# Optimization experiments

Hardware: AMD Instinct MI355X
Metric: run time of the kernel (lower is better)

## Reference

```python
import jax, jax.numpy as jnp
import numpy as np

D_MODEL = 768
N_HEADS = 12
HEAD_DIM = D_MODEL // N_HEADS


def setup_inputs() -> dict:
    key = jax.random.key(0)
    ks = jax.random.split(key, 9)
    s = 1.0 / np.sqrt(D_MODEL)
    return {
        "x": jax.random.normal(ks[0], (2, 2048, D_MODEL), dtype=jnp.float32),
        "Wq": jax.random.uniform(ks[1], (D_MODEL, D_MODEL), minval=-s, maxval=s, dtype=jnp.float32),
        "bq": jax.random.uniform(ks[2], (D_MODEL,), minval=-s, maxval=s, dtype=jnp.float32),
        "Wk": jax.random.uniform(ks[3], (D_MODEL, D_MODEL), minval=-s, maxval=s, dtype=jnp.float32),
        "bk": jax.random.uniform(ks[4], (D_MODEL,), minval=-s, maxval=s, dtype=jnp.float32),
        "Wv": jax.random.uniform(ks[5], (D_MODEL, D_MODEL), minval=-s, maxval=s, dtype=jnp.float32),
        "bv": jax.random.uniform(ks[6], (D_MODEL,), minval=-s, maxval=s, dtype=jnp.float32),
        "Wo": jax.random.uniform(ks[7], (D_MODEL, D_MODEL), minval=-s, maxval=s, dtype=jnp.float32),
        "bo": jax.random.uniform(ks[8], (D_MODEL,), minval=-s, maxval=s, dtype=jnp.float32),
    }


def reference(x, Wq, bq, Wk, bk, Wv, bv, Wo, bo):
    B, S, D = x.shape
    H, Hd = N_HEADS, HEAD_DIM
    # nn.Linear: y = x @ W.T + b
    q = (x @ Wq.T + bq).reshape(B, S, H, Hd).transpose(0, 2, 1, 3)  # [B,H,S,Hd]
    k = (x @ Wk.T + bk).reshape(B, S, H, Hd).transpose(0, 2, 1, 3)
    v = (x @ Wv.T + bv).reshape(B, S, H, Hd).transpose(0, 2, 1, 3)
    scores = jnp.einsum('bhqd,bhkd->bhqk', q, k) / np.sqrt(Hd)  # [B,H,S,S]
    attn = jax.nn.softmax(scores, axis=-1)
    out = jnp.einsum('bhqk,bhkd->bhqd', attn, v)  # [B,H,S,Hd]
    out = out.transpose(0, 2, 1, 3).reshape(B, S, D)
    return out @ Wo.T + bo
```

## Files before the change

### kernel.cpp

```cpp
#include <hip/hip_runtime.h>

#define D_MODEL 768
#define SEQ 2048
#define BATCH 2
#define NHEADS 12
#define HDIM 64
#define M_TOTAL (BATCH*SEQ)
#define NQK (2*D_MODEL)

typedef __attribute__((ext_vector_type(8))) short short8;
typedef __attribute__((ext_vector_type(4))) short short4_t;
typedef __attribute__((ext_vector_type(4))) float floatx4;

#define MFMA_PV(a,b,c) __builtin_amdgcn_mfma_f32_16x16x16bf16_1k(a,b,c,0,0,0)
#define EXP2(x) __builtin_amdgcn_exp2f(x)

static __device__ __forceinline__ unsigned short f2bf(float f) {
    union { float f; unsigned int u; } v; v.f = f;
    unsigned int r = (v.u + 0x7fffu + ((v.u >> 16) & 1u)) >> 16;
    return (unsigned short)r;
}

static __device__ __forceinline__ void async16(void* lds, const void* g) {
    __builtin_amdgcn_global_load_lds(
        (const __attribute__((address_space(1))) unsigned int*)g,
        (__attribute__((address_space(3))) unsigned int*)lds, 16, 0, 0);
}

#define X8    393216
#define W8    73728
#define CVT_N (X8 + 4*W8)
#define CVT_BLOCKS (CVT_N/256 + 6)
__global__ __launch_bounds__(256) void cvt_all_kernel(
    const float* __restrict__ x,  const float* __restrict__ Wq,
    const float* __restrict__ Wk, const float* __restrict__ Wv,
    const float* __restrict__ Wo, const float* __restrict__ bq,
    const float* __restrict__ bk,
    unsigned short* __restrict__ xb, unsigned short* __restrict__ wqk,
    unsigned short* __restrict__ wvb, unsigned short* __restrict__ wob,
    float* __restrict__ bqk)
{
    int i = blockIdx.x * 256 + threadIdx.x;
    if (i >= CVT_N) {
        int j = i - CVT_N;
        if (j < 1536) bqk[j] = (j < 768) ? bq[j] : bk[j - 768];
        return;
    }
    const float* src; unsigned short* dst;
    if (i < X8)             { src = x  + (size_t)i*8;            dst = xb  + (size_t)i*8; }
    else if (i < X8 + W8)   { int j = i - X8;          src = Wq + (size_t)j*8; dst = wqk + (size_t)j*8; }
    else if (i < X8 + 2*W8) { int j = i - (X8 + W8);   src = Wk + (size_t)j*8; dst = wqk + 589824 + (size_t)j*8; }
    else if (i < X8 + 3*W8) { int j = i - (X8 + 2*W8); src = Wv + (size_t)j*8; dst = wvb + (size_t)j*8; }
    else                    { int j = i - (X8 + 3*W8); src = Wo + (size_t)j*8; dst = wob + (size_t)j*8; }
    const float4* s = (const float4*)src;
    float4 a = s[0], b = s[1];
    short8 o;
    o[0]=(short)f2bf(a.x); o[1]=(short)f2bf(a.y); o[2]=(short)f2bf(a.z); o[3]=(short)f2bf(a.w);
    o[4]=(short)f2bf(b.x); o[5]=(short)f2bf(b.y); o[6]=(short)f2bf(b.z); o[7]=(short)f2bf(b.w);
    *(short8*)dst = o;
}

template<int MI>
__device__ __forceinline__ void gemm_core_db(
    const unsigned short* __restrict__ A, const unsigned short* __restrict__ W,
    int m0, int n0, unsigned short* smem, floatx4 (&acc)[MI][4], int t)
{
    const int ASZ = MI*32*64;
    const int BSZ = ASZ + 8192;
    const int quad = (t >> 4) & 3, l = t & 15;
    const int wvv = t >> 6, wr = wvv >> 1, wc = wvv & 1;
    const int base_off = t & ~63;

    auto stage = [&](int buf, int kt) {
        char* AsB = (char*)(smem + buf*BSZ);
        char* WsB = (char*)(smem + buf*BSZ + ASZ);
#pragma unroll
        for (int it = 0; it < MI; ++it) {
            int slot = it*256 + t;
            int r = slot >> 3, c = (slot & 7) ^ (r & 7);
            async16(AsB + (size_t)(it*256 + base_off)*16, A + (size_t)(m0+r)*768 + kt*64 + c*8);
        }
#pragma unroll
        for (int it = 0; it < 4; ++it) {
            int slot = it*256 + t;
            int r = slot >> 3, c = (slot & 7) ^ (r & 7);
            async16(WsB + (size_t)(it*256 + base_off)*16, W + (size_t)(n0+r)*768 + kt*64 + c*8);
        }
    };

    stage(0, 0);
    for (int kt = 0; kt < 12; ++kt) {
        __syncthreads();
        if (kt < 11) stage((kt+1)&1, kt+1);
        const char* AsB = (const char*)(smem + (kt&1)*BSZ);
        const char* WsB = (const char*)(smem + (kt&1)*BSZ + ASZ);
#pragma unroll
        for (int ks = 0; ks < 2; ++ks) {
            short8 af[MI], wf[4];
#pragma unroll
            for (int mi = 0; mi < MI; ++mi) {
                int m = wr*(MI*16) + mi*16 + l;
                af[mi] = *(const short8*)(AsB + m*128 + (((ks*4+quad) ^ (m&7))*16));
            }
#pragma unroll
            for (int ni = 0; ni < 4; ++ni) {
                int n = wc*64 + ni*16 + l;
                wf[ni] = *(const short8*)(WsB + n*128 + (((ks*4+quad) ^ (n&7))*16));
            }
#pragma unroll
            for (int mi = 0; mi < MI; ++mi)
#pragma unroll
                for (int ni = 0; ni < 4; ++ni)
                    acc[mi][ni] = __builtin_amdgcn_mfma_f32_16x16x32_bf16(
                        af[mi], wf[ni], acc[mi][ni], 0, 0, 0);
        }
    }
}

__global__ __launch_bounds__(256) void gemm_qkvt_kernel(
    const unsigned short* __restrict__ xb, const unsigned short* __restrict__ wqk,
    const unsigned short* __restrict__ wvb,
    const float* __restrict__ bqk, const float* __restrict__ bv,
    unsigned short* __restrict__ qkout, unsigned short* __restrict__ vtout)
{
    __shared__ unsigned short smem[2*16384];
    const int t = threadIdx.x;
    int bid = blockIdx.x;
    const bool isqk = bid < 384;
    const unsigned short *A, *W; int m0, n0;
    if (isqk) { A = xb;  W = wqk; m0 = (bid/12)*128; n0 = (bid%12)*128; }
    else { int v = bid - 384; A = wvb; W = xb; m0 = (v%6)*128; n0 = (v/6)*128; }

    floatx4 acc[4][4];
#pragma unroll
    for (int i=0;i<4;i++)
#pragma unroll
        for (int j=0;j<4;j++) acc[i][j] = (floatx4){0.f,0.f,0.f,0.f};

    gemm_core_db<4>(A, W, m0, n0, smem, acc, t);

    const int lane = t & 63, quad = lane >> 4, l = lane & 15;
    const int wvv = t >> 6, wr = wvv >> 1, wc = wvv & 1;

    __syncthreads();
#pragma unroll
    for (int mi=0;mi<4;mi++)
#pragma unroll
        for (int ni=0;ni<4;ni++) {
            int col = wc*64 + ni*16 + l;
            float bcol = isqk ? bqk[n0 + col] : 0.f;
#pragma unroll
            for (int r=0;r<4;r++) {
                int row = wr*64 + mi*16 + quad*4 + r;
                float bb = isqk ? bcol : bv[m0 + row];
                smem[row*128 + col] = f2bf(acc[mi][ni][r] + bb);
            }
        }
    __syncthreads();
#pragma unroll
    for (int i=0;i<8;i++) {
        int slot = i*256 + t;
        int r = slot >> 4, c = slot & 15;
        if (isqk) {
            short8 val = *(const short8*)(smem + r*128 + c*8);
            *(short8*)(qkout + (size_t)(m0+r)*NQK + n0 + c*8) = val;
        } else {
            int kb32 = (c >> 2)*32 + (c & 3)*4;
            short4_t lo = *(const short4_t*)(smem + r*128 + kb32);
            short4_t hi = *(const short4_t*)(smem + r*128 + kb32 + 16);
            short8 val;
            val[0]=lo[0]; val[1]=lo[1]; val[2]=lo[2]; val[3]=lo[3];
            val[4]=hi[0]; val[5]=hi[1]; val[6]=hi[2]; val[7]=hi[3];
            int f = m0 + r, tok = n0 + c*8;
            *(short8*)(vtout + ((size_t)(tok>>11)*768 + f)*SEQ + (tok & (SEQ-1))) = val;
        }
    }
}

__global__ __launch_bounds__(256) void gemm_out_kernel(
    const unsigned short* __restrict__ ab, const unsigned short* __restrict__ wob,
    const float* __restrict__ bo, float* __restrict__ out)
{
    __shared__ unsigned short smem[2*12288];
    const int t = threadIdx.x;
    int bid = blockIdx.x;
    int m0 = (bid/6)*64, n0 = (bid%6)*128;

    floatx4 acc[2][4];
#pragma unroll
    for (int i=0;i<2;i++)
#pragma unroll
        for (int j=0;j<4;j++) acc[i][j] = (floatx4){0.f,0.f,0.f,0.f};

    gemm_core_db<2>(ab, wob, m0, n0, smem, acc, t);

    const int lane = t & 63, quad = lane >> 4, l = lane & 15;
    const int wvv = t >> 6, wr = wvv >> 1, wc = wvv & 1;
#pragma unroll
    for (int mi=0;mi<2;mi++)
#pragma unroll
        for (int ni=0;ni<4;ni++) {
            int col = n0 + wc*64 + ni*16 + l;
            float bb = bo[col];
#pragma unroll
            for (int r=0;r<4;r++) {
                int row = m0 + wr*32 + mi*16 + quad*4 + r;
                out[(size_t)row*768 + col] = acc[mi][ni][r] + bb;
            }
        }
}

__global__ __launch_bounds__(256) void attn_kernel(
    const unsigned short* __restrict__ qk,
    const unsigned short* __restrict__ vt,
    unsigned short* __restrict__ aout)
{
    __shared__ unsigned short Ks[128*64];
    __shared__ unsigned short Vs[64*128];
    char* KsB = (char*)Ks; char* VsB = (char*)Vs;
    const int t = threadIdx.x;
    const int lane = t & 63, w = t >> 6;
    const int l16 = lane & 15, quad = lane >> 4;
    const int q0 = blockIdx.x * 64;
    const int h = blockIdx.y, b = blockIdx.z;
    const size_t rowbase = (size_t)b * SEQ;
    const size_t vbase = ((size_t)(b*NHEADS + h))*HDIM*SEQ;
    const int base_off = t & ~63;

    short8 qf0, qf1;
    {
        const unsigned short* qr = qk + (rowbase + q0 + w*16 + l16)*NQK + h*64;
        qf0 = *(const short8*)(qr + quad*8);
        qf1 = *(const short8*)(qr + 32 + quad*8);
    }

    floatx4 oacc[4];
#pragma unroll
    for (int i=0;i<4;i++) oacc[i] = (floatx4){0.f,0.f,0.f,0.f};
    float lsum = 0.f;
    short4_t pf[8];

    const float C1 = 0.18033688011112042f;
    const float C2 = -4.32808512266689f;

    for (int kt = 0; kt < SEQ/128; ++kt) {
        __syncthreads();
#pragma unroll
        for (int it = 0; it < 4; ++it) {
            int slot = it*256 + t;
            int r = slot >> 3, c = (slot & 7) ^ (r & 7);
            async16(KsB + (size_t)(it*256 + base_off)*16,
                    qk + (rowbase + kt*128 + r)*NQK + 768 + h*64 + c*8);
        }
#pragma unroll
        for (int it = 0; it < 4; ++it) {
            int slot = it*256 + t;
            int d = slot >> 4, c = (slot & 15) ^ (d & 15);
            async16(VsB + (size_t)(it*256 + base_off)*16,
                    vt + vbase + (size_t)d*SEQ + kt*128 + c*8);
        }
        __syncthreads();

#pragma unroll
        for (int mt = 0; mt < 8; ++mt) {
            int key = mt*16 + l16;
            short8 kf0 = *(const short8*)(KsB + key*128 + ((quad     ^ (l16&7))*16));
            short8 kf1 = *(const short8*)(KsB + key*128 + (((4+quad) ^ (l16&7))*16));
            floatx4 s = (floatx4){0.f,0.f,0.f,0.f};
            s = __builtin_amdgcn_mfma_f32_16x16x32_bf16(kf0, qf0, s, 0, 0, 0);
            s = __builtin_amdgcn_mfma_f32_16x16x32_bf16(kf1, qf1, s, 0, 0, 0);
            float p0 = EXP2(fmaf(s[0], C1, C2));
            float p1 = EXP2(fmaf(s[1], C1, C2));
            float p2 = EXP2(fmaf(s[2], C1, C2));
            float p3 = EXP2(fmaf(s[3], C1, C2));
            lsum += (p0 + p1) + (p2 + p3);
            short4_t pk;
            pk[0] = (short)f2bf(p0); pk[1] = (short)f2bf(p1);
            pk[2] = (short)f2bf(p2); pk[3] = (short)f2bf(p3);
            pf[mt] = pk;
        }

#pragma unroll
        for (int P = 0; P < 4; ++P) {
#pragma unroll
            for (int ni = 0; ni < 4; ++ni) {
                int row = ni*16 + l16;
                short8 vv = *(const short8*)(VsB + row*256 + (((P*4 + quad) ^ l16)*16));
                short4_t vlo = __builtin_shufflevector(vv, vv, 0, 1, 2, 3);
                short4_t vhi = __builtin_shufflevector(vv, vv, 4, 5, 6, 7);
                oacc[ni] = MFMA_PV(pf[2*P],     vlo, oacc[ni]);
                oacc[ni] = MFMA_PV(pf[2*P + 1], vhi, oacc[ni]);
            }
        }
    }

    lsum += __shfl_xor(lsum, 16);
    lsum += __shfl_xor(lsum, 32);
    float inv[4];
#pragma unroll
    for (int r = 0; r < 4; ++r)
        inv[r] = 1.0f / __shfl(lsum, quad*4 + r);

    __syncthreads();
    unsigned short* Ob = Ks;
#pragma unroll
    for (int ni = 0; ni < 4; ++ni)
#pragma unroll
        for (int r = 0; r < 4; ++r) {
            int row = w*16 + quad*4 + r;
            Ob[row*72 + ni*16 + l16] = f2bf(oacc[ni][r] * inv[r]);
        }
    __syncthreads();
#pragma unroll
    for (int it = 0; it < 2; ++it) {
        int slot = it*256 + t;
        int r = slot >> 3, c = slot & 7;
        *(short8*)(aout + (rowbase + q0 + r)*768 + h*64 + c*8) = *(const short8*)(Ob + r*72 + c*8);
    }
}

extern "C" void kernel_launch(void* const* d_in, const int* in_sizes, int n_in,
                              void* d_out, int out_size, void* d_ws, size_t ws_size,
                              hipStream_t stream)
{
    const float* x  = (const float*)d_in[0];
    const float* Wq = (const float*)d_in[1];
    const float* bq = (const float*)d_in[2];
    const float* Wk = (const float*)d_in[3];
    const float* bk = (const float*)d_in[4];
    const float* Wv = (const float*)d_in[5];
    const float* bv = (const float*)d_in[6];
    const float* Wo = (const float*)d_in[7];
    const float* bo = (const float*)d_in[8];

    unsigned short* ws = (unsigned short*)d_ws;
    unsigned short* xb  = ws;
    unsigned short* wqk = xb  + (size_t)3145728;
    unsigned short* wvb = wqk + (size_t)1179648;
    unsigned short* wob = wvb + (size_t)589824;
    unsigned short* qkb = wob + (size_t)589824;
    unsigned short* vtb = qkb + (size_t)6291456;
    unsigned short* ab  = vtb + (size_t)3145728;
    float* bqk = (float*)(ab + (size_t)3145728);

    cvt_all_kernel<<<CVT_BLOCKS, 256, 0, stream>>>(x, Wq, Wk, Wv, Wo, bq, bk,
                                                   xb, wqk, wvb, wob, bqk);

    gemm_qkvt_kernel<<<576, 256, 0, stream>>>(xb, wqk, wvb, bqk, bv, qkb, vtb);

    attn_kernel<<<dim3(SEQ/64, NHEADS, BATCH), 256, 0, stream>>>(qkb, vtb, ab);

    gemm_out_kernel<<<384, 256, 0, stream>>>(ab, wob, bo, (float*)d_out);
}
```

Baseline: 175.6 us.

## Halve GEMM K-tile, retile V and output GEMMs, reorder attention grid

The shared GEMM core now stages 32-wide K slices instead of 64-wide ones, with a new XOR swizzle and a second template parameter for the number of N sub-tiles. Shared memory per block drops, and launch bounds now request 2 or 4 blocks per CU. The V-projection uses 192x128 tiles (512 total QKV blocks), and the output GEMM uses 64x96 tiles (512 blocks). The attention grid puts heads on the fastest dimension, so blocks on the same query tile run together and can share cache. Each block gains occupancy and CU balance but does twice as many K iterations with more barriers.

```diff
diff --git a/kernel.cpp b/kernel.cpp
--- a/kernel.cpp
+++ b/kernel.cpp
@@ -60,13 +60,14 @@
     *(short8*)dst = o;
 }
 
-template<int MI>
-__device__ __forceinline__ void gemm_core_db(
+template<int MI, int NI>
+__device__ __forceinline__ void gemm_core32(
     const unsigned short* __restrict__ A, const unsigned short* __restrict__ W,
-    int m0, int n0, unsigned short* smem, floatx4 (&acc)[MI][4], int t)
-{
-    const int ASZ = MI*32*64;
-    const int BSZ = ASZ + 8192;
+    int m0, int n0, unsigned short* smem, floatx4 (&acc)[MI][NI], int t)
+{
+    const int ASZ = MI*32*32;
+    const int WSZ = NI*32*32;
+    const int BSZ = ASZ + WSZ;
     const int quad = (t >> 4) & 3, l = t & 15;
     const int wvv = t >> 6, wr = wvv >> 1, wc = wvv & 1;
     const int base_off = t & ~63;
@@ -75,96 +76,116 @@
         char* AsB = (char*)(smem + buf*BSZ);
         char* WsB = (char*)(smem + buf*BSZ + ASZ);
 #pragma unroll
-        for (int it = 0; it < MI; ++it) {
+        for (int it = 0; it < MI/2; ++it) {
             int slot = it*256 + t;
-            int r = slot >> 3, c = (slot & 7) ^ (r & 7);
-            async16(AsB + (size_t)(it*256 + base_off)*16, A + (size_t)(m0+r)*768 + kt*64 + c*8);
-        }
-#pragma unroll
-        for (int it = 0; it < 4; ++it) {
+            int r = slot >> 2, c = (slot & 3) ^ ((r >> 1) & 3);
+            async16(AsB + (size_t)(it*256 + base_off)*16, A + (size_t)(m0+r)*768 + kt*32 + c*8);
+        }
+#pragma unroll
+        for (int it = 0; it < (NI+1)/2; ++it) {
             int slot = it*256 + t;
-            int r = slot >> 3, c = (slot & 7) ^ (r & 7);
-            async16(WsB + (size_t)(it*256 + base_off)*16, W + (size_t)(n0+r)*768 + kt*64 + c*8);
+            if (slot < NI*128) {
+                int r = slot >> 2, c = (slot & 3) ^ ((r >> 1) & 3);
+                async16(WsB + (size_t)(it*256 + base_off)*16, W + (size_t)(n0+r)*768 + kt*32 + c*8);
+            }
         }
     };
 
     stage(0, 0);
-    for (int kt = 0; kt < 12; ++kt) {
-        __syncthreads();
-        if (kt < 11) stage((kt+1)&1, kt+1);
+    for (int kt = 0; kt < 24; ++kt) {
+        __syncthreads();
+        if (kt < 23) stage((kt+1)&1, kt+1);
         const char* AsB = (const char*)(smem + (kt&1)*BSZ);
         const char* WsB = (const char*)(smem + (kt&1)*BSZ + ASZ);
-#pragma unroll
-        for (int ks = 0; ks < 2; ++ks) {
-            short8 af[MI], wf[4];
-#pragma unroll
-            for (int mi = 0; mi < MI; ++mi) {
-                int m = wr*(MI*16) + mi*16 + l;
-                af[mi] = *(const short8*)(AsB + m*128 + (((ks*4+quad) ^ (m&7))*16));
-            }
-#pragma unroll
-            for (int ni = 0; ni < 4; ++ni) {
-                int n = wc*64 + ni*16 + l;
-                wf[ni] = *(const short8*)(WsB + n*128 + (((ks*4+quad) ^ (n&7))*16));
-            }
-#pragma unroll
-            for (int mi = 0; mi < MI; ++mi)
-#pragma unroll
-                for (int ni = 0; ni < 4; ++ni)
-                    acc[mi][ni] = __builtin_amdgcn_mfma_f32_16x16x32_bf16(
-                        af[mi], wf[ni], acc[mi][ni], 0, 0, 0);
-        }
-    }
-}
-
-__global__ __launch_bounds__(256) void gemm_qkvt_kernel(
+        short8 af[MI], wf[NI];
+#pragma unroll
+        for (int mi = 0; mi < MI; ++mi) {
+            int m = wr*(MI*16) + mi*16 + l;
+            af[mi] = *(const short8*)(AsB + m*64 + ((quad ^ ((m>>1)&3))*16));
+        }
+#pragma unroll
+        for (int ni = 0; ni < NI; ++ni) {
+            int n = wc*(NI*16) + ni*16 + l;
+            wf[ni] = *(const short8*)(WsB + n*64 + ((quad ^ ((n>>1)&3))*16));
+        }
+#pragma unroll
+        for (int mi = 0; mi < MI; ++mi)
+#pragma unroll
+            for (int ni = 0; ni < NI; ++ni)
+                acc[mi][ni] = __builtin_amdgcn_mfma_f32_16x16x32_bf16(
+                    af[mi], wf[ni], acc[mi][ni], 0, 0, 0);
+    }
+}
+
+__global__ __launch_bounds__(256, 2) void gemm_qkvt_kernel(
     const unsigned short* __restrict__ xb, const unsigned short* __restrict__ wqk,
     const unsigned short* __restrict__ wvb,
     const float* __restrict__ bqk, const float* __restrict__ bv,
     unsigned short* __restrict__ qkout, unsigned short* __restrict__ vtout)
 {
-    __shared__ unsigned short smem[2*16384];
+    __shared__ unsigned short smem[24576];
     const int t = threadIdx.x;
-    int bid = blockIdx.x;
-    const bool isqk = bid < 384;
-    const unsigned short *A, *W; int m0, n0;
-    if (isqk) { A = xb;  W = wqk; m0 = (bid/12)*128; n0 = (bid%12)*128; }
-    else { int v = bid - 384; A = wvb; W = xb; m0 = (v%6)*128; n0 = (v/6)*128; }
-
-    floatx4 acc[4][4];
-#pragma unroll
-    for (int i=0;i<4;i++)
-#pragma unroll
-        for (int j=0;j<4;j++) acc[i][j] = (floatx4){0.f,0.f,0.f,0.f};
-
-    gemm_core_db<4>(A, W, m0, n0, smem, acc, t);
-
+    const int bid = blockIdx.x;
     const int lane = t & 63, quad = lane >> 4, l = lane & 15;
-    const int wvv = t >> 6, wr = wvv >> 1, wc = wvv & 1;
-
-    __syncthreads();
-#pragma unroll
-    for (int mi=0;mi<4;mi++)
-#pragma unroll
-        for (int ni=0;ni<4;ni++) {
-            int col = wc*64 + ni*16 + l;
-            float bcol = isqk ? bqk[n0 + col] : 0.f;
-#pragma unroll
-            for (int r=0;r<4;r++) {
-                int row = wr*64 + mi*16 + quad*4 + r;
-                float bb = isqk ? bcol : bv[m0 + row];
-                smem[row*128 + col] = f2bf(acc[mi][ni][r] + bb);
-            }
-        }
-    __syncthreads();
-#pragma unroll
-    for (int i=0;i<8;i++) {
-        int slot = i*256 + t;
-        int r = slot >> 4, c = slot & 15;
-        if (isqk) {
+    const int wvv = t >> 6, wc = wvv & 1, wr = wvv >> 1;
+
+    if (bid < 384) {
+        int m0 = (bid/12)*128, n0 = (bid%12)*128;
+        floatx4 acc[4][4];
+#pragma unroll
+        for (int i=0;i<4;i++)
+#pragma unroll
+            for (int j=0;j<4;j++) acc[i][j] = (floatx4){0.f,0.f,0.f,0.f};
+        gemm_core32<4,4>(xb, wqk, m0, n0, smem, acc, t);
+
+        __syncthreads();
+#pragma unroll
+        for (int mi=0;mi<4;mi++)
+#pragma unroll
+            for (int ni=0;ni<4;ni++) {
+                int col = wc*64 + ni*16 + l;
+                float bcol = bqk[n0 + col];
+#pragma unroll
+                for (int r=0;r<4;r++) {
+                    int row = wr*64 + mi*16 + quad*4 + r;
+                    smem[row*128 + col] = f2bf(acc[mi][ni][r] + bcol);
+                }
+            }
+        __syncthreads();
+#pragma unroll
+        for (int i=0;i<8;i++) {
+            int slot = i*256 + t;
+            int r = slot >> 4, c = slot & 15;
             short8 val = *(const short8*)(smem + r*128 + c*8);
             *(short8*)(qkout + (size_t)(m0+r)*NQK + n0 + c*8) = val;
-        } else {
+        }
+    } else {
+        int v = bid - 384;
+        int m0 = (v & 3)*192, n0 = (v >> 2)*128;
+        floatx4 acc[6][4];
+#pragma unroll
+        for (int i=0;i<6;i++)
+#pragma unroll
+            for (int j=0;j<4;j++) acc[i][j] = (floatx4){0.f,0.f,0.f,0.f};
+        gemm_core32<6,4>(wvb, xb, m0, n0, smem, acc, t);
+
+        __syncthreads();
+#pragma unroll
+        for (int mi=0;mi<6;mi++)
+#pragma unroll
+            for (int ni=0;ni<4;ni++) {
+                int col = wc*64 + ni*16 + l;
+#pragma unroll
+                for (int r=0;r<4;r++) {
+                    int row = wr*96 + mi*16 + quad*4 + r;
+                    smem[row*128 + col] = f2bf(acc[mi][ni][r] + bv[m0 + row]);
+                }
+            }
+        __syncthreads();
+#pragma unroll
+        for (int i=0;i<12;i++) {
+            int slot = i*256 + t;
+            int r = slot >> 4, c = slot & 15;
             int kb32 = (c >> 2)*32 + (c & 3)*4;
             short4_t lo = *(const short4_t*)(smem + r*128 + kb32);
             short4_t hi = *(const short4_t*)(smem + r*128 + kb32 + 16);
@@ -177,30 +198,30 @@
     }
 }
 
-__global__ __launch_bounds__(256) void gemm_out_kernel(
+__global__ __launch_bounds__(256, 4) void gemm_out_kernel(
     const unsigned short* __restrict__ ab, const unsigned short* __restrict__ wob,
     const float* __restrict__ bo, float* __restrict__ out)
 {
-    __shared__ unsigned short smem[2*12288];
+    __shared__ unsigned short smem[2*5120];
     const int t = threadIdx.x;
     int bid = blockIdx.x;
-    int m0 = (bid/6)*64, n0 = (bid%6)*128;
-
-    floatx4 acc[2][4];
+    int m0 = (bid >> 3)*64, n0 = (bid & 7)*96;
+
+    floatx4 acc[2][3];
 #pragma unroll
     for (int i=0;i<2;i++)
 #pragma unroll
-        for (int j=0;j<4;j++) acc[i][j] = (floatx4){0.f,0.f,0.f,0.f};
-
-    gemm_core_db<2>(ab, wob, m0, n0, smem, acc, t);
+        for (int j=0;j<3;j++) acc[i][j] = (floatx4){0.f,0.f,0.f,0.f};
+
+    gemm_core32<2,3>(ab, wob, m0, n0, smem, acc, t);
 
     const int lane = t & 63, quad = lane >> 4, l = lane & 15;
     const int wvv = t >> 6, wr = wvv >> 1, wc = wvv & 1;
 #pragma unroll
     for (int mi=0;mi<2;mi++)
 #pragma unroll
-        for (int ni=0;ni<4;ni++) {
-            int col = n0 + wc*64 + ni*16 + l;
+        for (int ni=0;ni<3;ni++) {
+            int col = n0 + wc*48 + ni*16 + l;
             float bb = bo[col];
 #pragma unroll
             for (int r=0;r<4;r++) {
@@ -221,8 +242,9 @@
     const int t = threadIdx.x;
     const int lane = t & 63, w = t >> 6;
     const int l16 = lane & 15, quad = lane >> 4;
-    const int q0 = blockIdx.x * 64;
-    const int h = blockIdx.y, b = blockIdx.z;
+    const int h = blockIdx.x;
+    const int q0 = blockIdx.y * 64;
+    const int b = blockIdx.z;
     const size_t rowbase = (size_t)b * SEQ;
     const size_t vbase = ((size_t)(b*NHEADS + h))*HDIM*SEQ;
     const int base_off = t & ~63;
@@ -346,9 +368,9 @@
     cvt_all_kernel<<<CVT_BLOCKS, 256, 0, stream>>>(x, Wq, Wk, Wv, Wo, bq, bk,
                                                    xb, wqk, wvb, wob, bqk);
 
-    gemm_qkvt_kernel<<<576, 256, 0, stream>>>(xb, wqk, wvb, bqk, bv, qkb, vtb);
-
-    attn_kernel<<<dim3(SEQ/64, NHEADS, BATCH), 256, 0, stream>>>(qkb, vtb, ab);
-
-    gemm_out_kernel<<<384, 256, 0, stream>>>(ab, wob, bo, (float*)d_out);
-}
+    gemm_qkvt_kernel<<<512, 256, 0, stream>>>(xb, wqk, wvb, bqk, bv, qkb, vtb);
+
+    attn_kernel<<<dim3(NHEADS, SEQ/64, BATCH), 256, 0, stream>>>(qkb, vtb, ab);
+
+    gemm_out_kernel<<<512, 256, 0, stream>>>(ab, wob, bo, (float*)d_out);
+}
```

Measured after the change: 165.4 us. 5.8% less time.
